# Performance work log

Measured on AMD Instinct MI355X. Metric: run time of the kernel, lower is better.

Reference implementation:

```python
import jax, jax.numpy as jnp
import numpy as np

K_POS, K_NEG = 3, 2
MIN_D = 9  # min_dist=8 bumped to next odd, as in _nms_topk
BN_EPS = 1e-5


def _conv(x, w, pad):
    return jax.lax.conv_general_dilated(
        x, w, (1, 1), [(pad, pad), (pad, pad)],
        dimension_numbers=('NCHW', 'OIHW', 'NCHW'))


def _bn(x, g, b, m, v):
    scale = g * jax.lax.rsqrt(v + BN_EPS)  # inference-mode BN
    return x * scale[None, :, None, None] + (b - m * scale)[None, :, None, None]


def _head(x, w1, g1, b1, m1, v1, w2, g2, b2, m2, v2, w3, b3, out_hw):
    h = jax.nn.relu(_bn(_conv(x, w1, 1), g1, b1, m1, v1))
    h = jax.nn.relu(_bn(_conv(h, w2, 1), g2, b2, m2, v2))
    logits = _conv(h, w3, 0) + b3[None, :, None, None]
    B = logits.shape[0]
    # F.interpolate(mode='bilinear', align_corners=False) == half-pixel bilinear resize
    logits = jax.image.resize(logits, (B, 1, out_hw, out_hw), method='bilinear')
    return logits


def _sample_one(smap, key):
    # smap: [H, W] sigmoid heatmap for one sample
    H, W = smap.shape
    # --- positive points: NMS-style peak top-k ---
    local_max = jax.lax.reduce_window(
        smap, -jnp.inf, jax.lax.max, (MIN_D, MIN_D), (1, 1), 'SAME')
    is_peak = (smap == local_max) & (smap > 0.1)
    masked = jnp.where(is_peak, smap, -jnp.inf).reshape(-1)
    vals, idx = jax.lax.top_k(masked, K_POS)
    valid = jnp.isfinite(vals)  # slots corresponding to real peaks
    xs = jnp.where(valid, (idx % W).astype(jnp.float32), 0.0)
    ys = jnp.where(valid, (idx // W).astype(jnp.float32), 0.0)
    pos_lab = jnp.where(valid, 1, -1).astype(jnp.int32)
    # fallback: no peak at all -> single argmax point in slot 0
    amax = jnp.argmax(smap)
    any_peak = valid[0]
    xs = xs.at[0].set(jnp.where(any_peak, xs[0], (amax % W).astype(jnp.float32)))
    ys = ys.at[0].set(jnp.where(any_peak, ys[0], (amax // W).astype(jnp.float32)))
    pos_lab = pos_lab.at[0].set(1)  # slot 0 is always a positive point
    pos = jnp.stack([xs, ys], axis=1)  # [K_POS, 2] (x, y)
    # --- negative points: uniform sample from low-response region ---
    low = (smap < 0.3).reshape(-1)
    low_fb = (smap < smap.max()).reshape(-1)
    mask = jnp.where(jnp.any(low), low, low_fb)
    n = mask.sum()
    # stable argsort puts masked-in (True) flat indices first, in index order
    order = jnp.argsort(jnp.logical_not(mask))
    u = jax.random.uniform(key, (K_NEG,))
    ridx = jnp.minimum((u * jnp.maximum(n, 1).astype(jnp.float32)).astype(jnp.int32),
                       jnp.maximum(n - 1, 0))
    sel = order[ridx]
    neg = jnp.stack([sel % W, sel // W], axis=1).astype(jnp.float32)
    neg = jnp.where(n > 0, neg, jnp.zeros_like(neg))
    neg_lab = jnp.zeros((K_NEG,), jnp.int32)
    coords = jnp.concatenate([pos, neg], axis=0)      # [K_POS+K_NEG, 2]
    labels = jnp.concatenate([pos_lab, neg_lab], axis=0)
    return coords, labels


def setup_inputs() -> dict:
    key = jax.random.key(0)
    ks = jax.random.split(key, 4)
    B, C, h, w = 32, 256, 64, 64
    HID = 64
    x = jax.random.normal(ks[0], (B, C, h, w), jnp.float32)
    w1 = jax.random.normal(ks[1], (HID, C, 3, 3), jnp.float32) * 0.03  # kaiming-ish
    w2 = jax.random.normal(ks[2], (HID, HID, 3, 3), jnp.float32) * 0.06
    w3 = jax.random.normal(ks[3], (1, HID, 1, 1), jnp.float32) * 0.17
    b3 = jnp.full((1,), -2.0, jnp.float32)
    ones = jnp.ones((HID,), jnp.float32)
    zeros = jnp.zeros((HID,), jnp.float32)
    return {
        'encoder_features': x,
        'w1': w1, 'g1': ones, 'b1': zeros, 'm1': zeros, 'v1': ones,
        'w2': w2, 'g2': ones, 'b2': zeros, 'm2': zeros, 'v2': ones,
        'w3': w3, 'b3': b3,
        'output_size': 256,
    }


def reference(encoder_features, w1, g1, b1, m1, v1, w2, g2, b2, m2, v2, w3, b3, output_size):
    logits = _head(encoder_features, w1, g1, b1, m1, v1, w2, g2, b2, m2, v2, w3, b3, output_size)
    heatmap = jax.nn.sigmoid(logits)  # [B, 1, H, W]
    B = heatmap.shape[0]
    keys = jax.random.split(jax.random.key(42), B)
    coords, labels = jax.vmap(_sample_one)(heatmap[:, 0], keys)
    point_coords = coords[:, None].astype(jnp.float32)  # [B, 1, K, 2]
    point_labels = labels[:, None].astype(jnp.int32)    # [B, 1, K]
    return heatmap, point_coords, point_labels, logits
```

## Files before the change

### kernel.cpp

```cpp
#include <hip/hip_runtime.h>
#include <stdint.h>
#include <math.h>

#define NEG_INF (-__builtin_inff())
#define IDX_SENT 0x7fffffff

__device__ __forceinline__ void threefry2x32(uint32_t k0, uint32_t k1,
                                             uint32_t x0, uint32_t x1,
                                             uint32_t* o0, uint32_t* o1) {
  const uint32_t ks2 = k0 ^ k1 ^ 0x1BD11BDAu;
  uint32_t ks[3] = {k0, k1, ks2};
  const int rot[2][4] = {{13, 15, 26, 6}, {17, 29, 16, 24}};
  x0 += ks[0];
  x1 += ks[1];
#pragma unroll
  for (int i = 0; i < 5; ++i) {
#pragma unroll
    for (int j = 0; j < 4; ++j) {
      const int r = rot[i & 1][j];
      x0 += x1;
      x1 = (x1 << r) | (x1 >> (32 - r));
      x1 ^= x0;
    }
    x0 += ks[(i + 1) % 3];
    x1 += ks[(i + 2) % 3] + (uint32_t)(i + 1);
  }
  *o0 = x0;
  *o1 = x1;
}

__device__ __forceinline__ float bits_to_uniform(uint32_t bits) {
  return __uint_as_float((bits >> 9) | 0x3f800000u) - 1.0f;
}

__device__ __forceinline__ void top3_insert(float v, int idx, float tv[3], int ti[3]) {
  if ((v > tv[2]) || (v == tv[2] && idx < ti[2])) {
    tv[2] = v; ti[2] = idx;
    if ((tv[2] > tv[1]) || (tv[2] == tv[1] && ti[2] < ti[1])) {
      float fv = tv[1]; int fi = ti[1];
      tv[1] = tv[2]; ti[1] = ti[2];
      tv[2] = fv;     ti[2] = fi;
      if ((tv[1] > tv[0]) || (tv[1] == tv[0] && ti[1] < ti[0])) {
        fv = tv[0]; fi = ti[0];
        tv[0] = tv[1]; ti[0] = ti[1];
        tv[1] = fv;    ti[1] = fi;
      }
    }
  }
}

__global__ __launch_bounds__(256) void transpose_w4(
    const float* __restrict__ w, float* __restrict__ wt, int IC9) {
  const int idx = blockIdx.x * 256 + threadIdx.x;
  const int qrow = idx >> 6;
  const int oc = idx & 63;
  const float4 v = *(const float4*)&w[(size_t)oc * IC9 + qrow * 4];
  wt[(size_t)(qrow * 4 + 0) * 64 + oc] = v.x;
  wt[(size_t)(qrow * 4 + 1) * 64 + oc] = v.y;
  wt[(size_t)(qrow * 4 + 2) * 64 + oc] = v.z;
  wt[(size_t)(qrow * 4 + 3) * 64 + oc] = v.w;
}

template <int IC>
__global__ __launch_bounds__(512, 4) void conv3x3_bn_relu(
    const float* __restrict__ x, const float* __restrict__ wt,
    const float* __restrict__ g, const float* __restrict__ bb,
    const float* __restrict__ m, const float* __restrict__ vv,
    float* __restrict__ out) {
  __shared__ float xs[2][8][10][36];

  const int tid = threadIdx.x;
  const int blk = blockIdx.x;
  const int b = blk >> 4;
  const int tile = blk & 15;
  const int by = (tile >> 1) << 3;
  const int bx = (tile & 1) << 5;
  const int wv = __builtin_amdgcn_readfirstlane(tid >> 6);
  const int lane = tid & 63;
  const int r = lane & 7;
  const int lc = (lane >> 3) << 2;
  const int ocbase = wv << 3;

  const int sic = wv;
  const int sc = lane;
  const int gx = bx + sc - 1;
  const bool cok = (sc < 34) && (gx >= 0) && (gx < 64);

  float acc[4][8];
#pragma unroll
  for (int p = 0; p < 4; ++p)
#pragma unroll
    for (int o = 0; o < 8; ++o) acc[p][o] = 0.0f;

  float pre[10];
  {
    const float* xp = x + ((size_t)b * IC + sic) * 4096;
#pragma unroll
    for (int rr = 0; rr < 10; ++rr) {
      const int gy = by + rr - 1;
      pre[rr] = 0.0f;
      if (cok && gy >= 0 && gy < 64) pre[rr] = xp[gy * 64 + gx];
    }
#pragma unroll
    for (int rr = 0; rr < 10; ++rr)
      if (sc < 34) xs[0][sic][rr][sc] = pre[rr];
  }
  __syncthreads();

  int cur = 0;
  for (int icb = 0; icb < IC; icb += 8) {
    const bool has_next = (icb + 8) < IC;
    if (has_next) {
      const float* xp = x + ((size_t)b * IC + icb + 8 + sic) * 4096;
#pragma unroll
      for (int rr = 0; rr < 10; ++rr) {
        const int gy = by + rr - 1;
        pre[rr] = 0.0f;
        if (cok && gy >= 0 && gy < 64) pre[rr] = xp[gy * 64 + gx];
      }
    }

    const float* wbase = wt + (size_t)icb * 9 * 64 + ocbase;
    for (int ic = 0; ic < 8; ++ic) {
#pragma unroll
      for (int ky = 0; ky < 3; ++ky) {
        float xv[6];
        *(float4*)&xv[0] = *(const float4*)&xs[cur][ic][r + ky][lc];
        *(float2*)&xv[4] = *(const float2*)&xs[cur][ic][r + ky][lc + 4];
#pragma unroll
        for (int kx = 0; kx < 3; ++kx) {
          const float4* wp4 = (const float4*)(wbase + (ic * 9 + ky * 3 + kx) * 64);
#pragma unroll
          for (int q = 0; q < 2; ++q) {
            const float4 w4 = wp4[q];
#pragma unroll
            for (int p = 0; p < 4; ++p) {
              acc[p][4 * q + 0] = fmaf(xv[kx + p], w4.x, acc[p][4 * q + 0]);
              acc[p][4 * q + 1] = fmaf(xv[kx + p], w4.y, acc[p][4 * q + 1]);
              acc[p][4 * q + 2] = fmaf(xv[kx + p], w4.z, acc[p][4 * q + 2]);
              acc[p][4 * q + 3] = fmaf(xv[kx + p], w4.w, acc[p][4 * q + 3]);
            }
          }
        }
      }
    }

    if (has_next) {
#pragma unroll
      for (int rr = 0; rr < 10; ++rr)
        if (sc < 34) xs[cur ^ 1][sic][rr][sc] = pre[rr];
    }
    __syncthreads();
    cur ^= 1;
  }

#pragma unroll
  for (int o = 0; o < 8; ++o) {
    const int oc = ocbase + o;
    const float sc2 = g[oc] * (1.0f / sqrtf(vv[oc] + 1e-5f));
    const float sh = bb[oc] - m[oc] * sc2;
    float4 v;
    v.x = fmaxf(fmaf(acc[0][o], sc2, sh), 0.0f);
    v.y = fmaxf(fmaf(acc[1][o], sc2, sh), 0.0f);
    v.z = fmaxf(fmaf(acc[2][o], sc2, sh), 0.0f);
    v.w = fmaxf(fmaf(acc[3][o], sc2, sh), 0.0f);
    *(float4*)&out[(((size_t)b * 64 + oc) * 64 + (by + r)) * 64 + bx + lc] = v;
  }
}

__global__ __launch_bounds__(256) void logits64_k(
    const float* __restrict__ h2, const float* __restrict__ w3,
    const float* __restrict__ b3, float* __restrict__ lg64) {
  const int blk = blockIdx.x;
  const int b = blk >> 4;
  const int p = ((blk & 15) << 8) + threadIdx.x;
  __shared__ float wvv[64];
  if (threadIdx.x < 64) wvv[threadIdx.x] = w3[threadIdx.x];
  __syncthreads();
  float s = b3[0];
  const float* hp = h2 + (size_t)b * 64 * 4096 + p;
  for (int oc = 0; oc < 64; ++oc)
    s = fmaf(hp[(size_t)oc * 4096], wvv[oc], s);
  lg64[b * 4096 + p] = s;
}

__global__ __launch_bounds__(256) void upsample_k(
    const float* __restrict__ lg64, float* __restrict__ logits,
    float* __restrict__ heat) {
  const int blk = blockIdx.x;
  const int b = blk >> 6;
  const int qq = ((blk & 63) << 10) + (threadIdx.x << 2);
  const float* lg = lg64 + b * 4096;
  const int oy = qq >> 8;
  const float sy = (float)oy * 0.25f - 0.375f;
  const float fy = floorf(sy);
  const int y0 = (int)fy;
  const float ty = sy - fy;
  const int y0c = y0 < 0 ? 0 : y0;
  const int y1c = (y0 + 1) > 63 ? 63 : (y0 + 1);
  const float* r0 = lg + y0c * 64;
  const float* r1 = lg + y1c * 64;
  float4 lo, he;
  float* lop = (float*)&lo;
  float* hep = (float*)&he;
#pragma unroll
  for (int j = 0; j < 4; ++j) {
    const int ox = (qq & 255) + j;
    const float sx = (float)ox * 0.25f - 0.375f;
    const float fx = floorf(sx);
    const int x0 = (int)fx;
    const float tx = sx - fx;
    const int x0c = x0 < 0 ? 0 : x0;
    const int x1c = (x0 + 1) > 63 ? 63 : (x0 + 1);
    const float v00 = r0[x0c], v01 = r0[x1c];
    const float v10 = r1[x0c], v11 = r1[x1c];
    const float vtop = v00 + (v01 - v00) * tx;
    const float vbot = v10 + (v11 - v10) * tx;
    const float val = vtop + (vbot - vtop) * ty;
    lop[j] = val;
    hep[j] = 1.0f / (1.0f + expf(-val));
  }
  const size_t o = (size_t)b * 65536 + qq;
  *(float4*)(logits + o) = lo;
  *(float4*)(heat + o) = he;
}

__global__ __launch_bounds__(256) void pos_stripe(
    const float* __restrict__ heat, float* __restrict__ cand) {
  const int b = blockIdx.x >> 4;
  const int stripe = blockIdx.x & 15;
  const int y0 = stripe << 4;
  const float* s = heat + (size_t)b * 65536;
  const int tid = threadIdx.x;
  __shared__ float sm[24][256];
  __shared__ float rm[24][256];
  __shared__ float rv[256 * 3];
  __shared__ int ri[256 * 3];
  __shared__ float mvv[256];
  __shared__ int mii[256];
  __shared__ float rv2[24];
  __shared__ int ri2[24];
  __shared__ float mv2[8];
  __shared__ int mi2[8];

  for (int l = tid; l < 24 * 256; l += 256) {
    const int rr = l >> 8, xx = l & 255;
    const int gy = y0 - 4 + rr;
    sm[rr][xx] = (gy >= 0 && gy < 256) ? s[gy * 256 + xx] : NEG_INF;
  }
  __syncthreads();
  for (int l = tid; l < 24 * 256; l += 256) {
    const int rr = l >> 8, xx = l & 255;
    const int lo = (xx - 4 < 0) ? 0 : xx - 4;
    const int hi = (xx + 4 > 255) ? 255 : xx + 4;
    float mx = NEG_INF;
    for (int x2 = lo; x2 <= hi; ++x2) mx = fmaxf(mx, sm[rr][x2]);
    rm[rr][xx] = mx;
  }
  __syncthreads();

  float tv[3] = {NEG_INF, NEG_INF, NEG_INF};
  int ti[3] = {IDX_SENT, IDX_SENT, IDX_SENT};
  float bmax = NEG_INF;
  int bidx = IDX_SENT;
  for (int l = tid; l < 16 * 256; l += 256) {
    const int ry = l >> 8, xx = l & 255;
    const int lr = ry + 4;
    const float v = sm[lr][xx];
    float lm = rm[lr - 4][xx];
#pragma unroll
    for (int d = -3; d <= 4; ++d) lm = fmaxf(lm, rm[lr + d][xx]);
    const int gidx = (y0 + ry) * 256 + xx;
    if (v > bmax) { bmax = v; bidx = gidx; }
    if (v == lm && v > 0.1f) top3_insert(v, gidx, tv, ti);
  }

  rv[tid * 3 + 0] = tv[0]; rv[tid * 3 + 1] = tv[1]; rv[tid * 3 + 2] = tv[2];
  ri[tid * 3 + 0] = ti[0]; ri[tid * 3 + 1] = ti[1]; ri[tid * 3 + 2] = ti[2];
  mvv[tid] = bmax; mii[tid] = bidx;
  __syncthreads();

  if (tid < 8) {
    float av[3] = {NEG_INF, NEG_INF, NEG_INF};
    int ai[3] = {IDX_SENT, IDX_SENT, IDX_SENT};
    float am = NEG_INF; int amI = IDX_SENT;
    for (int t = tid * 32; t < tid * 32 + 32; ++t) {
      for (int k = 0; k < 3; ++k) top3_insert(rv[t * 3 + k], ri[t * 3 + k], av, ai);
      if (mvv[t] > am || (mvv[t] == am && mii[t] < amI)) { am = mvv[t]; amI = mii[t]; }
    }
    rv2[tid * 3 + 0] = av[0]; rv2[tid * 3 + 1] = av[1]; rv2[tid * 3 + 2] = av[2];
    ri2[tid * 3 + 0] = ai[0]; ri2[tid * 3 + 1] = ai[1]; ri2[tid * 3 + 2] = ai[2];
    mv2[tid] = am; mi2[tid] = amI;
  }
  __syncthreads();

  if (tid == 0) {
    float fv[3] = {NEG_INF, NEG_INF, NEG_INF};
    int fi[3] = {IDX_SENT, IDX_SENT, IDX_SENT};
    for (int t = 0; t < 24; ++t) top3_insert(rv2[t], ri2[t], fv, fi);
    float gbv = NEG_INF; int gbi = IDX_SENT;
    for (int t = 0; t < 8; ++t)
      if (mv2[t] > gbv || (mv2[t] == gbv && mi2[t] < gbi)) { gbv = mv2[t]; gbi = mi2[t]; }
    float* c = cand + ((size_t)b * 16 + stripe) * 8;
    c[0] = fv[0]; c[1] = __int_as_float(fi[0]);
    c[2] = fv[1]; c[3] = __int_as_float(fi[1]);
    c[4] = fv[2]; c[5] = __int_as_float(fi[2]);
    c[6] = gbv;   c[7] = __int_as_float(gbi);
  }
}

__global__ void pos_final(const float* __restrict__ cand,
                          float* __restrict__ coords, float* __restrict__ labels) {
  const int b = blockIdx.x;
  if (threadIdx.x != 0) return;
  float fv[3] = {NEG_INF, NEG_INF, NEG_INF};
  int fi[3] = {IDX_SENT, IDX_SENT, IDX_SENT};
  float gbv = NEG_INF; int gbi = IDX_SENT;
  for (int st = 0; st < 16; ++st) {
    const float* c = cand + ((size_t)b * 16 + st) * 8;
    for (int k = 0; k < 3; ++k)
      top3_insert(c[2 * k], __float_as_int(c[2 * k + 1]), fv, fi);
    const float mv = c[6]; const int mi = __float_as_int(c[7]);
    if (mv > gbv || (mv == gbv && mi < gbi)) { gbv = mv; gbi = mi; }
  }
  float* co = coords + (size_t)b * 10;
  float* la = labels + (size_t)b * 5;
  const bool any_peak = (fi[0] != IDX_SENT);
  const int i0 = any_peak ? fi[0] : gbi;
  co[0] = (float)(i0 & 255);
  co[1] = (float)(i0 >> 8);
  la[0] = 1.0f;
  for (int k = 1; k < 3; ++k) {
    const bool valid = (fi[k] != IDX_SENT);
    co[k * 2 + 0] = valid ? (float)(fi[k] & 255) : 0.0f;
    co[k * 2 + 1] = valid ? (float)(fi[k] >> 8) : 0.0f;
    la[k] = valid ? 1.0f : -1.0f;
  }
}

__global__ __launch_bounds__(256) void neg_count(
    const float* __restrict__ heat, float* __restrict__ ncnt,
    float* __restrict__ pmax) {
  const int blk = blockIdx.x;
  const int b = blk >> 2;
  const int part = blk & 3;
  const int tid = threadIdx.x;
  const int chunk = (part << 8) + tid;
  const float4* s = (const float4*)(heat + (size_t)b * 65536 + chunk * 64);
  int c = 0;
  float mx = NEG_INF;
  for (int i = 0; i < 16; ++i) {
    const float4 v = s[i];
    c += (v.x < 0.3f) + (v.y < 0.3f) + (v.z < 0.3f) + (v.w < 0.3f);
    mx = fmaxf(mx, fmaxf(fmaxf(v.x, v.y), fmaxf(v.z, v.w)));
  }
  ncnt[b * 1024 + chunk] = (float)c;
  __shared__ float mxs[256];
  mxs[tid] = mx;
  __syncthreads();
  if (tid == 0) {
    float gmx = NEG_INF;
    for (int t = 0; t < 256; ++t) gmx = fmaxf(gmx, mxs[t]);
    pmax[blk] = gmx;
  }
}

__global__ __launch_bounds__(256) void neg_select(
    const float* __restrict__ heat, const float* __restrict__ ncnt,
    const float* __restrict__ pmax, float* __restrict__ coords,
    float* __restrict__ labels) {
  const int b = blockIdx.x;
  const int tid = threadIdx.x;
  const float* s = heat + (size_t)b * 65536;
  __shared__ float cnt[1024];
  __shared__ float c256[256];
  __shared__ int pfx[257];
  __shared__ float thr_s;
  __shared__ int fb_s;
  __shared__ int n_s;
  __shared__ int ridx_s[2];

  for (int l = tid; l < 1024; l += 256) cnt[l] = ncnt[b * 1024 + l];
  __syncthreads();
  c256[tid] = cnt[4 * tid] + cnt[4 * tid + 1] + cnt[4 * tid + 2] + cnt[4 * tid + 3];
  __syncthreads();
  if (tid == 0) {
    int tot = 0;
    for (int t = 0; t < 256; ++t) tot += (int)c256[t];
    const float gm = fmaxf(fmaxf(pmax[b * 4], pmax[b * 4 + 1]),
                           fmaxf(pmax[b * 4 + 2], pmax[b * 4 + 3]));
    fb_s = (tot > 0) ? 0 : 1;
    thr_s = (tot > 0) ? 0.3f : gm;
  }
  __syncthreads();
  if (fb_s) {
    const float t2 = thr_s;
    const int base = tid * 256;
    int c = 0;
    for (int i = 0; i < 256; ++i) c += (s[base + i] < t2) ? 1 : 0;
    c256[tid] = (float)c;
    __syncthreads();
  }
  if (tid == 0) {
    int run = 0;
    for (int t = 0; t < 256; ++t) { pfx[t] = run; run += (int)c256[t]; }
    pfx[256] = run;
    const int n = run;
    n_s = n;
    uint32_t k0, k1, a0, a1;
    threefry2x32(0u, 42u, 0u, (uint32_t)b, &k0, &k1);
    threefry2x32(k0, k1, 0u, 0u, &a0, &a1);
    const uint32_t bits0 = a0 ^ a1;
    threefry2x32(k0, k1, 0u, 1u, &a0, &a1);
    const uint32_t bits1 = a0 ^ a1;
    const float u0 = bits_to_uniform(bits0);
    const float u1 = bits_to_uniform(bits1);
    const float nf = (float)(n > 1 ? n : 1);
    int r0 = (int)(u0 * nf);
    int r1 = (int)(u1 * nf);
    const int rmax = (n - 1 > 0) ? n - 1 : 0;
    ridx_s[0] = r0 < rmax ? r0 : rmax;
    ridx_s[1] = r1 < rmax ? r1 : rmax;
    labels[(size_t)b * 5 + 3] = 0.0f;
    labels[(size_t)b * 5 + 4] = 0.0f;
    if (n == 0) {
      coords[(size_t)b * 10 + 6] = 0.0f; coords[(size_t)b * 10 + 7] = 0.0f;
      coords[(size_t)b * 10 + 8] = 0.0f; coords[(size_t)b * 10 + 9] = 0.0f;
    }
  }
  __syncthreads();
  const int n = n_s;
  if (n > 0) {
    const float t2 = thr_s;
    const int p0 = pfx[tid], p1 = pfx[tid + 1];
    const int base = tid * 256;
    for (int j = 0; j < 2; ++j) {
      const int r = ridx_s[j];
      if (r >= p0 && r < p1) {
        int need = r - p0;
        int sel = -1;
        for (int i = 0; i < 256; ++i) {
          if (s[base + i] < t2) {
            if (need == 0) { sel = base + i; break; }
            --need;
          }
        }
        coords[(size_t)b * 10 + 6 + j * 2 + 0] = (float)(sel & 255);
        coords[(size_t)b * 10 + 6 + j * 2 + 1] = (float)(sel >> 8);
      }
    }
  }
}

extern "C" void kernel_launch(void* const* d_in, const int* in_sizes, int n_in,
                              void* d_out, int out_size, void* d_ws, size_t ws_size,
                              hipStream_t stream) {
  (void)in_sizes; (void)n_in; (void)out_size; (void)ws_size;
  const float* x  = (const float*)d_in[0];
  const float* w1 = (const float*)d_in[1];
  const float* g1 = (const float*)d_in[2];
  const float* b1 = (const float*)d_in[3];
  const float* m1 = (const float*)d_in[4];
  const float* v1 = (const float*)d_in[5];
  const float* w2 = (const float*)d_in[6];
  const float* g2 = (const float*)d_in[7];
  const float* b2 = (const float*)d_in[8];
  const float* m2 = (const float*)d_in[9];
  const float* v2 = (const float*)d_in[10];
  const float* w3 = (const float*)d_in[11];
  const float* b3 = (const float*)d_in[12];

  float* out = (float*)d_out;
  float* heat = out;
  float* coords = out + (size_t)32 * 65536;
  float* labels = coords + 320;
  float* logits = labels + 160;

  float* w1t = logits;
  float* w2t = logits + 147456;

  float* h1 = (float*)d_ws;
  float* h2 = h1 + (size_t)32 * 64 * 64 * 64;
  float* lg64 = h1;
  float* cand = h1 + 131072;
  float* ncnt = h1 + 135168;
  float* pmax = h1 + 167936;

  transpose_w4<<<144, 256, 0, stream>>>(w1, w1t, 2304);
  transpose_w4<<<36, 256, 0, stream>>>(w2, w2t, 576);
  conv3x3_bn_relu<256><<<512, 512, 0, stream>>>(x, w1t, g1, b1, m1, v1, h1);
  conv3x3_bn_relu<64><<<512, 512, 0, stream>>>(h1, w2t, g2, b2, m2, v2, h2);
  logits64_k<<<512, 256, 0, stream>>>(h2, w3, b3, lg64);
  upsample_k<<<2048, 256, 0, stream>>>(lg64, logits, heat);
  pos_stripe<<<512, 256, 0, stream>>>(heat, cand);
  pos_final<<<32, 64, 0, stream>>>(cand, coords, labels);
  neg_count<<<128, 256, 0, stream>>>(heat, ncnt, pmax);
  neg_select<<<32, 256, 0, stream>>>(heat, ncnt, pmax, coords, labels);
}
```

Measured before the change: 782.0 us.

## Split conv output channels across two blocks and stage input via global_load_lds

Each conv block now computes 32 output channels instead of 64, doubling the grid to 1024 blocks, and each thread holds a 2x8 accumulator tile instead of 4x8. Input tiles are copied straight from global memory into LDS with global_load_lds instead of passing through registers, and the buffers are zero-filled once so padding needs no explicit stores. The aim is more parallelism and less register pressure on a 512-block grid, at the cost of loading each input tile twice and doing fewer FMAs per LDS read. There is also a risk that no wait is issued on the asynchronous LDS loads before the barrier.

Result: slower. 830.8 us (+6.2%).

```diff
diff --git a/kernel.cpp b/kernel.cpp
--- a/kernel.cpp
+++ b/kernel.cpp
@@ -4,6 +4,9 @@
 
 #define NEG_INF (-__builtin_inff())
 #define IDX_SENT 0x7fffffff
+
+typedef __attribute__((address_space(1))) const void gas_t;
+typedef __attribute__((address_space(3))) void las_t;
 
 __device__ __forceinline__ void threefry2x32(uint32_t k0, uint32_t k1,
                                              uint32_t x0, uint32_t x1,
@@ -62,7 +65,7 @@
 }
 
 template <int IC>
-__global__ __launch_bounds__(512, 4) void conv3x3_bn_relu(
+__global__ __launch_bounds__(512, 3) void conv3x3_bn_relu(
     const float* __restrict__ x, const float* __restrict__ wt,
     const float* __restrict__ g, const float* __restrict__ bb,
     const float* __restrict__ m, const float* __restrict__ vv,
@@ -71,62 +74,63 @@
 
   const int tid = threadIdx.x;
   const int blk = blockIdx.x;
-  const int b = blk >> 4;
+  const int ocg = blk >> 9;
+  const int b = (blk >> 4) & 31;
   const int tile = blk & 15;
   const int by = (tile >> 1) << 3;
   const int bx = (tile & 1) << 5;
   const int wv = __builtin_amdgcn_readfirstlane(tid >> 6);
   const int lane = tid & 63;
-  const int r = lane & 7;
-  const int lc = (lane >> 3) << 2;
-  const int ocbase = wv << 3;
-
-  const int sic = wv;
+  const int rh = wv & 1;
+  const int os = wv >> 1;
+  const int r = (lane & 3) | (rh << 2);
+  const int lc = (lane >> 2) << 1;
+  const int ocbase = (ocg << 5) | (os << 3);
+
   const int sc = lane;
   const int gx = bx + sc - 1;
   const bool cok = (sc < 34) && (gx >= 0) && (gx < 64);
 
-  float acc[4][8];
-#pragma unroll
-  for (int p = 0; p < 4; ++p)
+  float acc[2][8];
+#pragma unroll
+  for (int p = 0; p < 2; ++p)
 #pragma unroll
     for (int o = 0; o < 8; ++o) acc[p][o] = 0.0f;
 
-  float pre[10];
-  {
-    const float* xp = x + ((size_t)b * IC + sic) * 4096;
-#pragma unroll
-    for (int rr = 0; rr < 10; ++rr) {
-      const int gy = by + rr - 1;
-      pre[rr] = 0.0f;
-      if (cok && gy >= 0 && gy < 64) pre[rr] = xp[gy * 64 + gx];
-    }
-#pragma unroll
-    for (int rr = 0; rr < 10; ++rr)
-      if (sc < 34) xs[0][sic][rr][sc] = pre[rr];
-  }
+  for (int l = tid; l < 2 * 8 * 10 * 36; l += 512)
+    (&xs[0][0][0][0])[l] = 0.0f;
+  __syncthreads();
+
+  auto stage = [&](int buf, int icb0) {
+    if (cok) {
+      const float* gb = x + ((size_t)b * IC + icb0 + wv) * 4096 + (by - 1) * 64 + gx;
+#pragma unroll
+      for (int rr = 0; rr < 10; ++rr) {
+        const int gy = by + rr - 1;
+        if (gy >= 0 && gy < 64) {
+          __builtin_amdgcn_global_load_lds(
+              (gas_t*)(const void*)(gb + rr * 64),
+              (las_t*)(void*)(&xs[buf][wv][rr][0]),
+              4, 0, 0);
+        }
+      }
+    }
+  };
+
+  stage(0, 0);
   __syncthreads();
 
   int cur = 0;
   for (int icb = 0; icb < IC; icb += 8) {
-    const bool has_next = (icb + 8) < IC;
-    if (has_next) {
-      const float* xp = x + ((size_t)b * IC + icb + 8 + sic) * 4096;
-#pragma unroll
-      for (int rr = 0; rr < 10; ++rr) {
-        const int gy = by + rr - 1;
-        pre[rr] = 0.0f;
-        if (cok && gy >= 0 && gy < 64) pre[rr] = xp[gy * 64 + gx];
-      }
-    }
+    if (icb + 8 < IC) stage(cur ^ 1, icb + 8);
 
     const float* wbase = wt + (size_t)icb * 9 * 64 + ocbase;
     for (int ic = 0; ic < 8; ++ic) {
 #pragma unroll
       for (int ky = 0; ky < 3; ++ky) {
-        float xv[6];
-        *(float4*)&xv[0] = *(const float4*)&xs[cur][ic][r + ky][lc];
-        *(float2*)&xv[4] = *(const float2*)&xs[cur][ic][r + ky][lc + 4];
+        float xv[4];
+        *(float2*)&xv[0] = *(const float2*)&xs[cur][ic][r + ky][lc];
+        *(float2*)&xv[2] = *(const float2*)&xs[cur][ic][r + ky][lc + 2];
 #pragma unroll
         for (int kx = 0; kx < 3; ++kx) {
           const float4* wp4 = (const float4*)(wbase + (ic * 9 + ky * 3 + kx) * 64);
@@ -134,7 +138,7 @@
           for (int q = 0; q < 2; ++q) {
             const float4 w4 = wp4[q];
 #pragma unroll
-            for (int p = 0; p < 4; ++p) {
+            for (int p = 0; p < 2; ++p) {
               acc[p][4 * q + 0] = fmaf(xv[kx + p], w4.x, acc[p][4 * q + 0]);
               acc[p][4 * q + 1] = fmaf(xv[kx + p], w4.y, acc[p][4 * q + 1]);
               acc[p][4 * q + 2] = fmaf(xv[kx + p], w4.z, acc[p][4 * q + 2]);
@@ -144,12 +148,6 @@
         }
       }
     }
-
-    if (has_next) {
-#pragma unroll
-      for (int rr = 0; rr < 10; ++rr)
-        if (sc < 34) xs[cur ^ 1][sic][rr][sc] = pre[rr];
-    }
     __syncthreads();
     cur ^= 1;
   }
@@ -159,12 +157,10 @@
     const int oc = ocbase + o;
     const float sc2 = g[oc] * (1.0f / sqrtf(vv[oc] + 1e-5f));
     const float sh = bb[oc] - m[oc] * sc2;
-    float4 v;
+    float2 v;
     v.x = fmaxf(fmaf(acc[0][o], sc2, sh), 0.0f);
     v.y = fmaxf(fmaf(acc[1][o], sc2, sh), 0.0f);
-    v.z = fmaxf(fmaf(acc[2][o], sc2, sh), 0.0f);
-    v.w = fmaxf(fmaf(acc[3][o], sc2, sh), 0.0f);
-    *(float4*)&out[(((size_t)b * 64 + oc) * 64 + (by + r)) * 64 + bx + lc] = v;
+    *(float2*)&out[(((size_t)b * 64 + oc) * 64 + (by + r)) * 64 + bx + lc] = v;
   }
 }
 
@@ -488,8 +484,8 @@
 
   transpose_w4<<<144, 256, 0, stream>>>(w1, w1t, 2304);
   transpose_w4<<<36, 256, 0, stream>>>(w2, w2t, 576);
-  conv3x3_bn_relu<256><<<512, 512, 0, stream>>>(x, w1t, g1, b1, m1, v1, h1);
-  conv3x3_bn_relu<64><<<512, 512, 0, stream>>>(h1, w2t, g2, b2, m2, v2, h2);
+  conv3x3_bn_relu<256><<<1024, 512, 0, stream>>>(x, w1t, g1, b1, m1, v1, h1);
+  conv3x3_bn_relu<64><<<1024, 512, 0, stream>>>(h1, w2t, g2, b2, m2, v2, h2);
   logits64_k<<<512, 256, 0, stream>>>(h2, w3, b3, lg64);
   upsample_k<<<2048, 256, 0, stream>>>(lg64, logits, heat);
   pos_stripe<<<512, 256, 0, stream>>>(heat, cand);
```
